# Optimization experiments

Hardware: AMD Instinct MI355X
Metric: run time of the kernel (lower is better)

## Reference

```python
import jax, jax.numpy as jnp
import numpy as np

N_PER_G = 100  # nodes per graph


def setup_inputs() -> dict:
    key = jax.random.key(0)
    ks = jax.random.split(key, 12)
    N, G, E = 100000, 1000, 1600000
    ninp, nout, K, H, H2 = 3, 10, 5, 64, 32
    x = jax.random.normal(ks[0], (N, ninp), jnp.float32)
    # within-graph random edges (contiguous node blocks per graph)
    epg = E // G
    gid = jnp.arange(E, dtype=jnp.int32) // epg
    src = jax.random.randint(ks[1], (E,), 0, N_PER_G, jnp.int32) + gid * N_PER_G
    dst = jax.random.randint(ks[2], (E,), 0, N_PER_G, jnp.int32) + gid * N_PER_G
    edge_index = jnp.stack([src, dst])
    batch = (jnp.arange(N, dtype=jnp.int32) // N_PER_G)
    lambda_max = 1.5 + 0.5 * jax.random.uniform(ks[3], (G,), jnp.float32)
    s = 0.05
    W1 = jax.random.normal(ks[4], (K, ninp, H), jnp.float32) * s
    b1 = jnp.zeros((H,), jnp.float32)
    W2 = jax.random.normal(ks[5], (K, H, H), jnp.float32) * s
    b2 = jnp.zeros((H,), jnp.float32)
    W3 = jax.random.normal(ks[6], (K, H, H), jnp.float32) * s
    b3 = jnp.zeros((H,), jnp.float32)
    bn_gamma = jnp.ones((H,), jnp.float32)
    bn_beta = jnp.zeros((H,), jnp.float32)
    bn_mean = jnp.zeros((H,), jnp.float32)
    bn_var = jnp.ones((H,), jnp.float32)
    fc1_w = jax.random.normal(ks[7], (H, H2), jnp.float32) * s
    fc1_b = jnp.zeros((H2,), jnp.float32)
    fc2_w = jax.random.normal(ks[8], (H2, nout), jnp.float32) * s
    fc2_b = jnp.zeros((nout,), jnp.float32)
    return dict(x=x, edge_index=edge_index, batch=batch, lambda_max=lambda_max,
                W1=W1, b1=b1, W2=W2, b2=b2, W3=W3, b3=b3,
                bn_gamma=bn_gamma, bn_beta=bn_beta, bn_mean=bn_mean, bn_var=bn_var,
                fc1_w=fc1_w, fc1_b=fc1_b, fc2_w=fc2_w, fc2_b=fc2_b)


def _cheb_conv(x, W, b, row, col, coef_edge, coef_loop):
    # PyG ChebConv with sym-normalized scaled Laplacian:
    # Lhat x = scatter_add(coef_edge * x[col] -> row) + coef_loop * x
    N = x.shape[0]
    def lhat(h):
        return jax.ops.segment_sum(coef_edge[:, None] * h[col], row,
                                   num_segments=N) + coef_loop[:, None] * h
    Tx0 = x
    out = Tx0 @ W[0]
    Tx1 = lhat(x)
    out = out + Tx1 @ W[1]
    for k in range(2, W.shape[0]):
        Tx2 = 2.0 * lhat(Tx1) - Tx0
        out = out + Tx2 @ W[k]
        Tx0, Tx1 = Tx1, Tx2
    return out + b


def reference(x, edge_index, batch, lambda_max,
              W1, b1, W2, b2, W3, b3,
              bn_gamma, bn_beta, bn_mean, bn_var,
              fc1_w, fc1_b, fc2_w, fc2_b):
    N = x.shape[0]
    G = lambda_max.shape[0]
    row, col = edge_index[0], edge_index[1]
    # sym Laplacian normalization, scaled by 2/lambda_max (per-graph)
    deg = jax.ops.segment_sum(jnp.ones_like(row, dtype=x.dtype), row, num_segments=N)
    dis = jnp.where(deg > 0, deg, 1.0) ** -0.5
    dis = jnp.where(deg > 0, dis, 0.0)
    lmax_e = lambda_max[batch[row]]
    coef_edge = -(2.0 / lmax_e) * dis[row] * dis[col]   # off-diagonal of Lhat
    coef_loop = 2.0 / lambda_max[batch] - 1.0           # diagonal of Lhat
    h = jax.nn.relu(_cheb_conv(x, W1, b1, row, col, coef_edge, coef_loop))
    h = jax.nn.relu(_cheb_conv(h, W2, b2, row, col, coef_edge, coef_loop))
    h = jax.nn.relu(_cheb_conv(h, W3, b3, row, col, coef_edge, coef_loop))
    # global mean pool over graphs
    sums = jax.ops.segment_sum(h, batch, num_segments=G)
    cnts = jax.ops.segment_sum(jnp.ones((N,), h.dtype), batch, num_segments=G)
    g = sums / jnp.maximum(cnts, 1.0)[:, None]
    # BatchNorm1d (eval mode, running stats), eps=1e-5
    g = (g - bn_mean) * jax.lax.rsqrt(bn_var + 1e-5) * bn_gamma + bn_beta
    g = jax.nn.relu(g @ fc1_w + fc1_b)
    return jax.nn.log_softmax(g @ fc2_w + fc2_b, axis=1)
```

## Files before the change

kernel.cpp:

```cpp
#include <hip/hip_runtime.h>

#define NPG 100
#define HF 64
#define NROW 128
#define ST 72
#define SAT 136
#define CMW 28

typedef float  f4   __attribute__((ext_vector_type(4)));
typedef float  f16v __attribute__((ext_vector_type(16)));
typedef short  bf8  __attribute__((ext_vector_type(8)));

#define SZ_TC  (HF * SAT * 2)
#define SZ_TRM (NROW * ST * 2)
#define OFF_TC  0
#define OFF_TRM SZ_TC
#define OFF_CM  0
#define OFF_MISC (OFF_TRM + SZ_TRM)
#define SMEM_BYTES (OFF_MISC + 1280)

#define WT_TOTAL 46080

__device__ __forceinline__ unsigned short f2bf(float f) {
    unsigned u = __float_as_uint(f);
    u += 0x7fffu + ((u >> 16) & 1u);
    return (unsigned short)(u >> 16);
}
__device__ __forceinline__ float bf2f(unsigned short h) {
    return __uint_as_float(((unsigned)h) << 16);
}
__device__ __forceinline__ f16v zerov16() {
    f16v z;
    #pragma unroll
    for (int i = 0; i < 16; i++) z[i] = 0.f;
    return z;
}

__global__ void wconv(const float* __restrict__ W1, const float* __restrict__ W2,
                      const float* __restrict__ W3, unsigned short* __restrict__ ws)
{
    int idx = blockIdx.x * 256 + threadIdx.x;
    if (idx >= WT_TOTAL) return;
    float v;
    if (idx < 5120) {
        int k5 = idx >> 10, rem = idx & 1023, fo = rem >> 4, fi = rem & 15;
        v = (fi < 3) ? W1[(k5 * 3 + fi) * HF + fo] : 0.f;
    } else if (idx < 25600) {
        int j = idx - 5120;
        int k5 = j >> 12, rem = j & 4095, fo = rem >> 6, fi = rem & 63;
        v = W2[(k5 * HF + fi) * HF + fo];
    } else {
        int j = idx - 25600;
        int k5 = j >> 12, rem = j & 4095, fo = rem >> 6, fi = rem & 63;
        v = W3[(k5 * HF + fi) * HF + fo];
    }
    ws[idx] = f2bf(v);
}

__launch_bounds__(256, 2)
__global__ void chebreg(const float* __restrict__ x, const int* __restrict__ ei,
                        const float* __restrict__ lambda_max,
                        const unsigned short* __restrict__ Wt,
                        const float* __restrict__ b1, const float* __restrict__ b2,
                        const float* __restrict__ b3,
                        const float* __restrict__ bng, const float* __restrict__ bnb,
                        const float* __restrict__ bnm, const float* __restrict__ bnv,
                        const float* __restrict__ fc1w, const float* __restrict__ fc1b,
                        const float* __restrict__ fc2w, const float* __restrict__ fc2b,
                        float* __restrict__ out, int E_total, int epg)
{
    extern __shared__ char sm[];
    const int tid = threadIdx.x;
    const int g = blockIdx.x;
    const int ebase = g * epg, nbase = g * NPG;
    const int wg = tid >> 6, lane = tid & 63;
    const int l31 = lane & 31, hh = lane >> 5;
    const int ht  = wg & 1;
    const int Mt0 = (wg >> 1) * 2;
    const int fo  = ht * 32 + l31;

    unsigned* Cm  = (unsigned*)(sm + OFF_CM);
    float* dis    = (float*)(sm + OFF_MISC);
    float* pool   = (float*)(sm + OFF_MISC + 448);
    float* gvn    = (float*)(sm + OFF_MISC + 704);
    float* zf     = (float*)(sm + OFF_MISC + 960);
    float* logits = (float*)(sm + OFF_MISC + 1088);
    float* lsep   = (float*)(sm + OFF_MISC + 1152);

    const float lam = lambda_max[g];
    const float two_l = 2.0f / lam;
    const float cl = two_l - 1.0f;

    for (int i = tid; i < (NROW * CMW) / 4; i += 256)
        ((f4*)Cm)[i] = (f4){0.f, 0.f, 0.f, 0.f};
    __syncthreads();
    for (int e = tid; e < epg; e += 256) {
        int r = ei[ebase + e] - nbase;
        int c = ei[E_total + ebase + e] - nbase;
        atomicAdd(&Cm[r * CMW + (c >> 2)], 1u << (8 * (c & 3)));
    }
    __syncthreads();
    if (tid < 112) {
        float dv = 0.f;
        if (tid < NPG) {
            unsigned s = 0;
            #pragma unroll
            for (int w = 0; w < CMW; w++) {
                unsigned u = Cm[tid * CMW + w];
                s += (u & 255) + ((u >> 8) & 255) + ((u >> 16) & 255) + (u >> 24);
            }
            dv = s > 0 ? rsqrtf((float)s) : 0.f;
        }
        dis[tid] = dv;
    }
    __syncthreads();

    bf8 af[2][7];
    #pragma unroll
    for (int m = 0; m < 2; m++) {
        int rr = 32 * (Mt0 + m) + l31;
        bool rv = (rr < NPG);
        float base = rv ? (-two_l * dis[rr]) : 0.f;
        #pragma unroll
        for (int Ks = 0; Ks < 7; Ks++) {
            int k0 = Ks * 16 + 8 * hh;
            unsigned w0 = rv ? Cm[rr * CMW + (k0 >> 2)]     : 0u;
            unsigned w1 = rv ? Cm[rr * CMW + (k0 >> 2) + 1] : 0u;
            #pragma unroll
            for (int j = 0; j < 8; j++) {
                int k = k0 + j;
                unsigned cnt = (((j < 4) ? w0 : w1) >> (8 * (k & 3))) & 255u;
                float v = base * (float)cnt * dis[k];
                if (rv && k == rr) v += cl;
                af[m][Ks][j] = (short)f2bf(v);
            }
        }
    }
    __syncthreads();

    for (int i = tid; i < (SZ_TC + SZ_TRM) / 16; i += 256)
        ((f4*)sm)[i] = (f4){0.f, 0.f, 0.f, 0.f};
    if (tid < HF) pool[tid] = 0.f;
    __syncthreads();
    if (tid < NPG) {
        unsigned short h0 = f2bf(x[(nbase + tid) * 3 + 0]);
        unsigned short h1 = f2bf(x[(nbase + tid) * 3 + 1]);
        unsigned short h2 = f2bf(x[(nbase + tid) * 3 + 2]);
        *(unsigned*)(sm + OFF_TRM + (tid * ST) * 2) = (unsigned)h0 | ((unsigned)h1 << 16);
        *(unsigned short*)(sm + OFF_TRM + (tid * ST + 2) * 2) = h2;
        *(unsigned short*)(sm + OFF_TC + (0 * SAT + tid) * 2) = h0;
        *(unsigned short*)(sm + OFF_TC + (1 * SAT + tid) * 2) = h1;
        *(unsigned short*)(sm + OFF_TC + (2 * SAT + tid) * 2) = h2;
    }
    __syncthreads();

    f16v acc[2];
    unsigned prev[2][8], oldr[2][8];
    const float* bsv[3] = {b1, b2, b3};

    for (int L = 0; L < 3; L++) {
        const bool l1 = (L == 0);
        const unsigned short* Wl = l1 ? Wt : (Wt + (L == 1 ? 5120 : 25600));
        acc[0] = zerov16();
        acc[1] = zerov16();

        #pragma unroll
        for (int m = 0; m < 2; m++) {
            unsigned short tv[16];
            #pragma unroll
            for (int r = 0; r < 16; r++) {
                int np = (Mt0 + m) * 32 + (r & 3) + 8 * (r >> 2) + 4 * hh;
                tv[r] = *(const unsigned short*)(sm + OFF_TRM + (np * ST + fo) * 2);
            }
            #pragma unroll
            for (int p = 0; p < 8; p++)
                prev[m][p] = (unsigned)tv[2 * p] | ((unsigned)tv[2 * p + 1] << 16);
        }

        auto TW = [&](int k5) {
            const int nKs = l1 ? 1 : 4;
            for (int Ks = 0; Ks < nKs; Ks++) {
                bf8 bw;
                if (l1) bw = *(const bf8*)(Wl + (k5 * 64 + fo) * 16 + 8 * hh);
                else    bw = *(const bf8*)(Wl + (k5 * 64 + fo) * 64 + Ks * 16 + 8 * hh);
                #pragma unroll
                for (int m = 0; m < 2; m++) {
                    bf8 a = *(const bf8*)(sm + OFF_TRM +
                              (((Mt0 + m) * 32 + l31) * ST + Ks * 16 + 8 * hh) * 2);
                    acc[m] = __builtin_amdgcn_mfma_f32_32x32x16_bf16(a, bw, acc[m], 0, 0, 0);
                }
            }
        };

        TW(0);
        for (int s = 1; s <= 4; s++) {
            bf8 bfr[7];
            #pragma unroll
            for (int Ks = 0; Ks < 7; Ks++)
                bfr[Ks] = *(const bf8*)(sm + OFF_TC +
                            (fo * SAT + Ks * 16 + 8 * hh) * 2);
            __syncthreads();
            #pragma unroll
            for (int m = 0; m < 2; m++) {
                f16v c = zerov16();
                #pragma unroll
                for (int Ks = 0; Ks < 7; Ks++)
                    c = __builtin_amdgcn_mfma_f32_32x32x16_bf16(af[m][Ks], bfr[Ks], c, 0, 0, 0);
                unsigned short h[16];
                #pragma unroll
                for (int r = 0; r < 16; r++) {
                    float v = c[r];
                    if (s >= 2) {
                        unsigned short o = (unsigned short)
                            ((oldr[m][r >> 1] >> (16 * (r & 1))) & 0xffff);
                        v = 2.f * v - bf2f(o);
                    }
                    h[r] = f2bf(v);
                }
                #pragma unroll
                for (int p = 0; p < 8; p++) {
                    oldr[m][p] = prev[m][p];
                    prev[m][p] = (unsigned)h[2 * p] | ((unsigned)h[2 * p + 1] << 16);
                }
                #pragma unroll
                for (int q4 = 0; q4 < 4; q4++) {
                    int np0 = (Mt0 + m) * 32 + 8 * q4 + 4 * hh;
                    uint2 pk;
                    pk.x = prev[m][2 * q4];
                    pk.y = prev[m][2 * q4 + 1];
                    *(uint2*)(sm + OFF_TC + (fo * SAT + np0) * 2) = pk;
                }
                #pragma unroll
                for (int r = 0; r < 16; r++) {
                    int np = (Mt0 + m) * 32 + (r & 3) + 8 * (r >> 2) + 4 * hh;
                    *(unsigned short*)(sm + OFF_TRM + (np * ST + fo) * 2) = h[r];
                }
            }
            __syncthreads();
            TW(s);
        }
        __syncthreads();

        const float bias = bsv[L][fo];
        if (L < 2) {
            #pragma unroll
            for (int m = 0; m < 2; m++) {
                unsigned short h[16];
                #pragma unroll
                for (int r = 0; r < 16; r++) {
                    h[r] = f2bf(fmaxf(acc[m][r] + bias, 0.f));
                    int np = (Mt0 + m) * 32 + (r & 3) + 8 * (r >> 2) + 4 * hh;
                    *(unsigned short*)(sm + OFF_TRM + (np * ST + fo) * 2) = h[r];
                }
                #pragma unroll
                for (int q4 = 0; q4 < 4; q4++) {
                    int np0 = (Mt0 + m) * 32 + 8 * q4 + 4 * hh;
                    uint2 pk;
                    pk.x = (unsigned)h[4 * q4]     | ((unsigned)h[4 * q4 + 1] << 16);
                    pk.y = (unsigned)h[4 * q4 + 2] | ((unsigned)h[4 * q4 + 3] << 16);
                    *(uint2*)(sm + OFF_TC + (fo * SAT + np0) * 2) = pk;
                }
            }
            __syncthreads();
        } else {
            float ssum = 0.f;
            #pragma unroll
            for (int m = 0; m < 2; m++) {
                #pragma unroll
                for (int r = 0; r < 16; r++) {
                    int np = (Mt0 + m) * 32 + (r & 3) + 8 * (r >> 2) + 4 * hh;
                    float h = fmaxf(acc[m][r] + bias, 0.f);
                    if (np < NPG) ssum += h;
                }
            }
            ssum += __shfl_xor(ssum, 32, 64);
            if (hh == 0) atomicAdd(&pool[fo], ssum);
            __syncthreads();
        }
    }

    if (tid < HF) {
        float gv = pool[tid] * (1.0f / NPG);
        gv = (gv - bnm[tid]) * rsqrtf(bnv[tid] + 1e-5f) * bng[tid] + bnb[tid];
        gvn[tid] = gv;
    }
    __syncthreads();
    if (tid < 32) {
        float a = fc1b[tid];
        for (int f = 0; f < HF; f++) a += gvn[f] * fc1w[f * 32 + tid];
        zf[tid] = fmaxf(a, 0.f);
    }
    __syncthreads();
    if (tid < 10) {
        float a = fc2b[tid];
        for (int k = 0; k < 32; k++) a += zf[k] * fc2w[k * 10 + tid];
        logits[tid] = a;
    }
    __syncthreads();
    if (tid == 0) {
        float m = logits[0];
        for (int i = 1; i < 10; i++) m = fmaxf(m, logits[i]);
        float s = 0.f;
        for (int i = 0; i < 10; i++) s += expf(logits[i] - m);
        lsep[0] = m + logf(s);
    }
    __syncthreads();
    if (tid < 10) out[g * 10 + tid] = logits[tid] - lsep[0];
}

extern "C" void kernel_launch(void* const* d_in, const int* in_sizes, int n_in,
                              void* d_out, int out_size, void* d_ws, size_t ws_size,
                              hipStream_t stream) {
    const float* x    = (const float*)d_in[0];
    const int*   ei   = (const int*)d_in[1];
    const float* lmax = (const float*)d_in[3];
    const float* W1   = (const float*)d_in[4];
    const float* b1   = (const float*)d_in[5];
    const float* W2   = (const float*)d_in[6];
    const float* b2   = (const float*)d_in[7];
    const float* W3   = (const float*)d_in[8];
    const float* b3   = (const float*)d_in[9];
    const float* bng  = (const float*)d_in[10];
    const float* bnb  = (const float*)d_in[11];
    const float* bnm  = (const float*)d_in[12];
    const float* bnv  = (const float*)d_in[13];
    const float* fc1w = (const float*)d_in[14];
    const float* fc1b = (const float*)d_in[15];
    const float* fc2w = (const float*)d_in[16];
    const float* fc2b = (const float*)d_in[17];

    const int E = in_sizes[1] / 2;
    const int G = in_sizes[3];
    const int epg = E / G;

    unsigned short* Wt = (unsigned short*)d_ws;

    wconv<<<(WT_TOTAL + 255) / 256, 256, 0, stream>>>(W1, W2, W3, Wt);

    hipFuncSetAttribute((const void*)chebreg,
                        hipFuncAttributeMaxDynamicSharedMemorySize, SMEM_BYTES);

    chebreg<<<G, 256, SMEM_BYTES, stream>>>(x, ei, lmax, Wt, b1, b2, b3,
                                            bng, bnb, bnm, bnv, fc1w, fc1b, fc2w, fc2b,
                                            (float*)d_out, E, epg);
}
```

Before: 172.0 us.

## Double-buffer Chebyshev LDS tiles to drop a barrier per step

Adds a second pair of LDS buffers for the transposed and row-major Chebyshev terms and ping-pongs between them across recursion steps and layers. This removes the barrier that guarded in-place overwrites and lets the weight-projection MFMAs be issued alongside the Laplacian MFMAs in the same phase. Per-layer register state is carried forward instead of reloaded from LDS. LDS use per block roughly doubles, which could constrain occupancy.

```diff
diff --git a/kernel.cpp b/kernel.cpp
--- a/kernel.cpp
+++ b/kernel.cpp
@@ -13,10 +13,12 @@
 
 #define SZ_TC  (HF * SAT * 2)
 #define SZ_TRM (NROW * ST * 2)
-#define OFF_TC  0
-#define OFF_TRM SZ_TC
-#define OFF_CM  0
-#define OFF_MISC (OFF_TRM + SZ_TRM)
+#define OFF_TC0  0
+#define OFF_TRM0 SZ_TC
+#define OFF_TC1  (OFF_TRM0 + SZ_TRM)
+#define OFF_TRM1 (OFF_TC1 + SZ_TC)
+#define OFF_CM   0
+#define OFF_MISC (OFF_TRM1 + SZ_TRM)
 #define SMEM_BYTES (OFF_MISC + 1280)
 
 #define WT_TOTAL 46080
@@ -58,16 +60,16 @@
 }
 
 __launch_bounds__(256, 2)
-__global__ void chebreg(const float* __restrict__ x, const int* __restrict__ ei,
-                        const float* __restrict__ lambda_max,
-                        const unsigned short* __restrict__ Wt,
-                        const float* __restrict__ b1, const float* __restrict__ b2,
-                        const float* __restrict__ b3,
-                        const float* __restrict__ bng, const float* __restrict__ bnb,
-                        const float* __restrict__ bnm, const float* __restrict__ bnv,
-                        const float* __restrict__ fc1w, const float* __restrict__ fc1b,
-                        const float* __restrict__ fc2w, const float* __restrict__ fc2b,
-                        float* __restrict__ out, int E_total, int epg)
+__global__ void chebpp(const float* __restrict__ x, const int* __restrict__ ei,
+                       const float* __restrict__ lambda_max,
+                       const unsigned short* __restrict__ Wt,
+                       const float* __restrict__ b1, const float* __restrict__ b2,
+                       const float* __restrict__ b3,
+                       const float* __restrict__ bng, const float* __restrict__ bnb,
+                       const float* __restrict__ bnm, const float* __restrict__ bnv,
+                       const float* __restrict__ fc1w, const float* __restrict__ fc1b,
+                       const float* __restrict__ fc2w, const float* __restrict__ fc2b,
+                       float* __restrict__ out, int E_total, int epg)
 {
     extern __shared__ char sm[];
     const int tid = threadIdx.x;
@@ -146,11 +148,11 @@
         unsigned short h0 = f2bf(x[(nbase + tid) * 3 + 0]);
         unsigned short h1 = f2bf(x[(nbase + tid) * 3 + 1]);
         unsigned short h2 = f2bf(x[(nbase + tid) * 3 + 2]);
-        *(unsigned*)(sm + OFF_TRM + (tid * ST) * 2) = (unsigned)h0 | ((unsigned)h1 << 16);
-        *(unsigned short*)(sm + OFF_TRM + (tid * ST + 2) * 2) = h2;
-        *(unsigned short*)(sm + OFF_TC + (0 * SAT + tid) * 2) = h0;
-        *(unsigned short*)(sm + OFF_TC + (1 * SAT + tid) * 2) = h1;
-        *(unsigned short*)(sm + OFF_TC + (2 * SAT + tid) * 2) = h2;
+        *(unsigned*)(sm + OFF_TRM0 + (tid * ST) * 2) = (unsigned)h0 | ((unsigned)h1 << 16);
+        *(unsigned short*)(sm + OFF_TRM0 + (tid * ST + 2) * 2) = h2;
+        *(unsigned short*)(sm + OFF_TC0 + (0 * SAT + tid) * 2) = h0;
+        *(unsigned short*)(sm + OFF_TC0 + (1 * SAT + tid) * 2) = h1;
+        *(unsigned short*)(sm + OFF_TC0 + (2 * SAT + tid) * 2) = h2;
     }
     __syncthreads();
 
@@ -158,26 +160,30 @@
     unsigned prev[2][8], oldr[2][8];
     const float* bsv[3] = {b1, b2, b3};
 
+    #pragma unroll
+    for (int m = 0; m < 2; m++) {
+        unsigned short tv[16];
+        #pragma unroll
+        for (int r = 0; r < 16; r++) {
+            int np = (Mt0 + m) * 32 + (r & 3) + 8 * (r >> 2) + 4 * hh;
+            tv[r] = *(const unsigned short*)(sm + OFF_TRM0 + (np * ST + fo) * 2);
+        }
+        #pragma unroll
+        for (int p = 0; p < 8; p++)
+            prev[m][p] = (unsigned)tv[2 * p] | ((unsigned)tv[2 * p + 1] << 16);
+    }
+
+    int pc = 0;
     for (int L = 0; L < 3; L++) {
         const bool l1 = (L == 0);
         const unsigned short* Wl = l1 ? Wt : (Wt + (L == 1 ? 5120 : 25600));
         acc[0] = zerov16();
         acc[1] = zerov16();
 
-        #pragma unroll
-        for (int m = 0; m < 2; m++) {
-            unsigned short tv[16];
-            #pragma unroll
-            for (int r = 0; r < 16; r++) {
-                int np = (Mt0 + m) * 32 + (r & 3) + 8 * (r >> 2) + 4 * hh;
-                tv[r] = *(const unsigned short*)(sm + OFF_TRM + (np * ST + fo) * 2);
-            }
-            #pragma unroll
-            for (int p = 0; p < 8; p++)
-                prev[m][p] = (unsigned)tv[2 * p] | ((unsigned)tv[2 * p + 1] << 16);
-        }
-
-        auto TW = [&](int k5) {
+        int tS_tc = pc ? OFF_TC1 : OFF_TC0,  tS_tr = pc ? OFF_TRM1 : OFF_TRM0;
+        int tD_tc = pc ? OFF_TC0 : OFF_TC1,  tD_tr = pc ? OFF_TRM0 : OFF_TRM1;
+
+        auto TW = [&](int trOff, int k5) {
             const int nKs = l1 ? 1 : 4;
             for (int Ks = 0; Ks < nKs; Ks++) {
                 bf8 bw;
@@ -185,21 +191,20 @@
                 else    bw = *(const bf8*)(Wl + (k5 * 64 + fo) * 64 + Ks * 16 + 8 * hh);
                 #pragma unroll
                 for (int m = 0; m < 2; m++) {
-                    bf8 a = *(const bf8*)(sm + OFF_TRM +
+                    bf8 a = *(const bf8*)(sm + trOff +
                               (((Mt0 + m) * 32 + l31) * ST + Ks * 16 + 8 * hh) * 2);
                     acc[m] = __builtin_amdgcn_mfma_f32_32x32x16_bf16(a, bw, acc[m], 0, 0, 0);
                 }
             }
         };
 
-        TW(0);
+        #pragma unroll
         for (int s = 1; s <= 4; s++) {
             bf8 bfr[7];
             #pragma unroll
             for (int Ks = 0; Ks < 7; Ks++)
-                bfr[Ks] = *(const bf8*)(sm + OFF_TC +
-                            (fo * SAT + Ks * 16 + 8 * hh) * 2);
-            __syncthreads();
+                bfr[Ks] = *(const bf8*)(sm + tS_tc + (fo * SAT + Ks * 16 + 8 * hh) * 2);
+            TW(tS_tr, s - 1);
             #pragma unroll
             for (int m = 0; m < 2; m++) {
                 f16v c = zerov16();
@@ -228,18 +233,19 @@
                     uint2 pk;
                     pk.x = prev[m][2 * q4];
                     pk.y = prev[m][2 * q4 + 1];
-                    *(uint2*)(sm + OFF_TC + (fo * SAT + np0) * 2) = pk;
+                    *(uint2*)(sm + tD_tc + (fo * SAT + np0) * 2) = pk;
                 }
                 #pragma unroll
                 for (int r = 0; r < 16; r++) {
                     int np = (Mt0 + m) * 32 + (r & 3) + 8 * (r >> 2) + 4 * hh;
-                    *(unsigned short*)(sm + OFF_TRM + (np * ST + fo) * 2) = h[r];
+                    *(unsigned short*)(sm + tD_tr + (np * ST + fo) * 2) = h[r];
                 }
             }
             __syncthreads();
-            TW(s);
-        }
-        __syncthreads();
+            int t = tS_tc; tS_tc = tD_tc; tD_tc = t;
+            t = tS_tr; tS_tr = tD_tr; tD_tr = t;
+        }
+        TW(tS_tr, 4);
 
         const float bias = bsv[L][fo];
         if (L < 2) {
@@ -250,18 +256,22 @@
                 for (int r = 0; r < 16; r++) {
                     h[r] = f2bf(fmaxf(acc[m][r] + bias, 0.f));
                     int np = (Mt0 + m) * 32 + (r & 3) + 8 * (r >> 2) + 4 * hh;
-                    *(unsigned short*)(sm + OFF_TRM + (np * ST + fo) * 2) = h[r];
-                }
+                    *(unsigned short*)(sm + tD_tr + (np * ST + fo) * 2) = h[r];
+                }
+                #pragma unroll
+                for (int p = 0; p < 8; p++)
+                    prev[m][p] = (unsigned)h[2 * p] | ((unsigned)h[2 * p + 1] << 16);
                 #pragma unroll
                 for (int q4 = 0; q4 < 4; q4++) {
                     int np0 = (Mt0 + m) * 32 + 8 * q4 + 4 * hh;
                     uint2 pk;
-                    pk.x = (unsigned)h[4 * q4]     | ((unsigned)h[4 * q4 + 1] << 16);
-                    pk.y = (unsigned)h[4 * q4 + 2] | ((unsigned)h[4 * q4 + 3] << 16);
-                    *(uint2*)(sm + OFF_TC + (fo * SAT + np0) * 2) = pk;
+                    pk.x = prev[m][2 * q4];
+                    pk.y = prev[m][2 * q4 + 1];
+                    *(uint2*)(sm + tD_tc + (fo * SAT + np0) * 2) = pk;
                 }
             }
             __syncthreads();
+            pc ^= 1;
         } else {
             float ssum = 0.f;
             #pragma unroll
@@ -337,10 +347,10 @@
 
     wconv<<<(WT_TOTAL + 255) / 256, 256, 0, stream>>>(W1, W2, W3, Wt);
 
-    hipFuncSetAttribute((const void*)chebreg,
+    hipFuncSetAttribute((const void*)chebpp,
                         hipFuncAttributeMaxDynamicSharedMemorySize, SMEM_BYTES);
 
-    chebreg<<<G, 256, SMEM_BYTES, stream>>>(x, ei, lmax, Wt, b1, b2, b3,
-                                            bng, bnb, bnm, bnv, fc1w, fc1b, fc2w, fc2b,
-                                            (float*)d_out, E, epg);
-}
+    chebpp<<<G, 256, SMEM_BYTES, stream>>>(x, ei, lmax, Wt, b1, b2, b3,
+                                           bng, bnb, bnm, bnv, fc1w, fc1b, fc2w, fc2b,
+                                           (float*)d_out, E, epg);
+}
```

After: 287.8 us. 1.67x slower.
